# Performance work log

Measured on AMD Instinct MI355X. Metric: run time of the kernel, lower is better.

The kernel has to match this reference:

```python
import jax, jax.numpy as jnp
import numpy as np

NUM_NODES = 512
NUM_EDGES = 512
EMB_DIM = 128
HIDDEN = 256
NUM_INC = 8192


def setup_inputs() -> dict:
    key = jax.random.key(0)
    ks = jax.random.split(key, 8)
    X = jax.random.normal(ks[0], (NUM_NODES, EMB_DIM), dtype=jnp.float32)
    V = jax.random.randint(ks[1], (NUM_INC,), 0, NUM_NODES, dtype=jnp.int64)
    E = jax.random.randint(ks[2], (NUM_INC,), 0, NUM_EDGES, dtype=jnp.int64)
    # MLP params, torch nn.Linear layout: W (out, in), y = x @ W.T + b
    lim1 = 1.0 / np.sqrt(2 * EMB_DIM)
    W1 = jax.random.uniform(ks[3], (HIDDEN, 2 * EMB_DIM), minval=-lim1, maxval=lim1, dtype=jnp.float32)
    b1 = jax.random.uniform(ks[4], (HIDDEN,), minval=-lim1, maxval=lim1, dtype=jnp.float32)
    lim2 = 1.0 / np.sqrt(HIDDEN)
    W2 = jax.random.uniform(ks[5], (1, HIDDEN), minval=-lim2, maxval=lim2, dtype=jnp.float32)
    b2 = jax.random.uniform(ks[6], (1,), minval=-lim2, maxval=lim2, dtype=jnp.float32)
    return {"X": X, "V": V, "E": E, "W1": W1, "b1": b1, "W2": W2, "b2": b2}


def reference(X, V, E, W1, b1, W2, b2):
    d = X.shape[-1]
    # scatter-mean of gathered node embeddings into edges; empty edges -> 0 (nan_to_num)
    sums = jax.ops.segment_sum(X[V], E, num_segments=NUM_EDGES)          # (M, d)
    cnt = jax.ops.segment_sum(jnp.ones((V.shape[0],), X.dtype), E, num_segments=NUM_EDGES)
    eX = jnp.where(cnt[:, None] > 0, sums / jnp.maximum(cnt[:, None], 1.0), 0.0)
    # cat([X_expanded, eX_expanded]) @ W1.T == X @ W1[:, :d].T + eX @ W1[:, d:].T (broadcast add)
    hX = X @ W1[:, :d].T                                                 # (N, H)
    hE = eX @ W1[:, d:].T                                                # (M, H)
    hidden = jax.nn.relu(hX[:, None, :] + hE[None, :, :] + b1)           # (N, M, H)
    logits = jnp.einsum('nmh,h->nm', hidden, W2[0]) + b2[0]              # (N, M)
    prob = jax.nn.sigmoid(logits)
    prob = jnp.nan_to_num(prob, nan=0.5)
    prob = jnp.clip(prob, 1e-6, 1.0 - 1e-6)
    return prob
```

## Files before the change

kernel.cpp:

```cpp
#include <hip/hip_runtime.h>
#include <math.h>

#define NN 512
#define MM 512
#define DD 128
#define HH 256

typedef float     v4f __attribute__((ext_vector_type(4)));
typedef _Float16  h8  __attribute__((ext_vector_type(8)));
typedef _Float16  h2  __attribute__((ext_vector_type(2)));


__global__ __launch_bounds__(256) void k_stage(
    const float* __restrict__ X, const int* __restrict__ V,
    const int* __restrict__ E, const float* __restrict__ W1,
    const float* __restrict__ b1, _Float16* __restrict__ A,
    _Float16* __restrict__ C, int ninc)
{
    __shared__ union {
        int    lst[8192];
        float4 w1t[64][32];
    } u;
    __shared__ float xr[4][128];
    __shared__ float red[16][64];
    __shared__ int   cnt4[4], pos4[4], off4[4];

    const int b = blockIdx.x;
    const int t = threadIdx.x;
    const int w = t >> 6, lane = t & 63;
    const bool edge = (b < 128);

    if (edge) {
        const int e0 = b * 4;
        if (t < 4) { cnt4[t] = 0; pos4[t] = 0; }
        __syncthreads();
        const int nq = ninc >> 2;
        for (int c = t; c < nq; c += 256) {
            int4 e4 = ((const int4*)E)[c];
            if ((unsigned)(e4.x - e0) < 4u) atomicAdd(&cnt4[e4.x - e0], 1);
            if ((unsigned)(e4.y - e0) < 4u) atomicAdd(&cnt4[e4.y - e0], 1);
            if ((unsigned)(e4.z - e0) < 4u) atomicAdd(&cnt4[e4.z - e0], 1);
            if ((unsigned)(e4.w - e0) < 4u) atomicAdd(&cnt4[e4.w - e0], 1);
        }
        __syncthreads();
        if (t == 0) {
            off4[0] = 0;
            off4[1] = cnt4[0];
            off4[2] = cnt4[0] + cnt4[1];
            off4[3] = off4[2] + cnt4[2];
        }
        __syncthreads();
        for (int c = t; c < nq; c += 256) {
            int4 e4 = ((const int4*)E)[c];
            int4 v4 = ((const int4*)V)[c];
            if ((unsigned)(e4.x - e0) < 4u) u.lst[off4[e4.x-e0] + atomicAdd(&pos4[e4.x-e0], 1)] = v4.x;
            if ((unsigned)(e4.y - e0) < 4u) u.lst[off4[e4.y-e0] + atomicAdd(&pos4[e4.y-e0], 1)] = v4.y;
            if ((unsigned)(e4.z - e0) < 4u) u.lst[off4[e4.z-e0] + atomicAdd(&pos4[e4.z-e0], 1)] = v4.z;
            if ((unsigned)(e4.w - e0) < 4u) u.lst[off4[e4.w-e0] + atomicAdd(&pos4[e4.w-e0], 1)] = v4.w;
        }
        __syncthreads();
        const int cnt = cnt4[w], off = off4[w];
        float s0a=0.f,s0b=0.f,s0c=0.f,s0d=0.f, s1a=0.f,s1b=0.f,s1c=0.f,s1d=0.f;
        int j = 0;
        for (; j + 4 <= cnt; j += 4) {
            int v0 = u.lst[off+j], v1 = u.lst[off+j+1], v2 = u.lst[off+j+2], v3 = u.lst[off+j+3];
            s0a += X[v0*DD + lane];      s1a += X[v0*DD + 64 + lane];
            s0b += X[v1*DD + lane];      s1b += X[v1*DD + 64 + lane];
            s0c += X[v2*DD + lane];      s1c += X[v2*DD + 64 + lane];
            s0d += X[v3*DD + lane];      s1d += X[v3*DD + 64 + lane];
        }
        for (; j < cnt; ++j) {
            int v = u.lst[off+j];
            s0a += X[v*DD + lane];       s1a += X[v*DD + 64 + lane];
        }
        float inv = cnt > 0 ? 1.0f / (float)cnt : 0.0f;
        xr[w][lane]      = (s0a+s0b+s0c+s0d) * inv;
        xr[w][lane+64]   = (s1a+s1b+s1c+s1d) * inv;
        __syncthreads();
    } else {
        const int r0 = (b - 128) * 4;
        ((float*)xr)[t]       = X[r0*DD + t];
        ((float*)xr)[t + 256] = X[r0*DD + 256 + t];
        __syncthreads();
    }

    const int r0row = edge ? b*4 : (b-128)*4;
    const int koff  = edge ? DD : 0;
    _Float16* Out   = edge ? C : A;

    #pragma unroll 1
    for (int p = 0; p < 4; ++p) {
        const int h0 = p * 64;
        #pragma unroll
        for (int q = 0; q < 8; ++q) {
            int c  = q * 256 + t;
            int h  = c >> 5, kq = c & 31;
            u.w1t[h][kq ^ (h & 31)] =
                *(const float4*)&W1[(h0 + h) * (2*DD) + koff + kq * 4];
        }
        __syncthreads();
        v4f acc0 = (v4f)(0.f), acc1 = (v4f)(0.f), acc2 = (v4f)(0.f), acc3 = (v4f)(0.f);
        #pragma unroll
        for (int i = 0; i < 8; ++i) {
            int kq = w * 8 + i;
            v4f wv = *(const v4f*)&u.w1t[lane][kq ^ (lane & 31)];
            acc0 += wv * (*(const v4f*)&xr[0][kq*4]);
            acc1 += wv * (*(const v4f*)&xr[1][kq*4]);
            acc2 += wv * (*(const v4f*)&xr[2][kq*4]);
            acc3 += wv * (*(const v4f*)&xr[3][kq*4]);
        }
        red[w*4 + 0][lane] = acc0.x + acc0.y + acc0.z + acc0.w;
        red[w*4 + 1][lane] = acc1.x + acc1.y + acc1.z + acc1.w;
        red[w*4 + 2][lane] = acc2.x + acc2.y + acc2.z + acc2.w;
        red[w*4 + 3][lane] = acc3.x + acc3.y + acc3.z + acc3.w;
        __syncthreads();
        float s = red[w][lane] + red[4 + w][lane] + red[8 + w][lane] + red[12 + w][lane];
        if (edge) s += b1[h0 + lane];
        Out[(r0row + w) * HH + h0 + lane] = (_Float16)s;
        __syncthreads();
    }
}

#define CT 8192
#define WT 16384

__device__ inline float dot8(h8 w, h8 a, h8 c, float acc) {
    h8 s = a + c;
    s = __builtin_elementwise_max(s, (h8)(_Float16)0.f);
    union { h8 v; h2 p[4]; } su, wu;
    su.v = s; wu.v = w;
    acc = __builtin_amdgcn_fdot2(su.p[0], wu.p[0], acc, false);
    acc = __builtin_amdgcn_fdot2(su.p[1], wu.p[1], acc, false);
    acc = __builtin_amdgcn_fdot2(su.p[2], wu.p[2], acc, false);
    acc = __builtin_amdgcn_fdot2(su.p[3], wu.p[3], acc, false);
    return acc;
}

__global__ __launch_bounds__(256) void k_pairs(
    const _Float16* __restrict__ A, const _Float16* __restrict__ C,
    const float* __restrict__ W2, const float* __restrict__ b2,
    float* __restrict__ out)
{
    __shared__ _Float16 lds[WT + 256];
    const int t  = threadIdx.x;
    const int bx = blockIdx.x;
    const int tn0 = (bx >> 4) * 32;
    const int tm0 = (bx & 15) * 32;

    lds[WT + t] = (_Float16)W2[t];
    #pragma unroll
    for (int q = 0; q < 8; ++q) {
        int g   = q * 256 + t;
        int row = g >> 5, cc = g & 31, r = row & 31;
        int dst = (row < 32 ? 0 : CT) + r * 256 + ((cc ^ (r >> 2)) << 3);
        const _Float16* src = (row < 32) ? A + (tn0 + r) * HH + cc * 8
                                         : C + (tm0 + r) * HH + cc * 8;
        *(h8*)&lds[dst] = *(const h8*)src;
    }
    __syncthreads();

    const int w  = t >> 6, lane = t & 63;
    const int qa = lane & 7,  ra = 4 * qa;
    const int qc = lane >> 3, rc = 4 * qc;
    const int h0 = w * 64;

    float acc[4][4];
    #pragma unroll
    for (int i = 0; i < 4; ++i)
        #pragma unroll
        for (int j = 0; j < 4; ++j) acc[i][j] = 0.f;

    #pragma unroll
    for (int hh = 0; hh < 64; hh += 8) {
        int h  = h0 + hh;
        int cc = h >> 3;
        int sa = (cc ^ qa) << 3;
        int sc = (cc ^ qc) << 3;
        h8 wv = *(const h8*)&lds[WT + h];
        h8 av[4], cv[4];
        #pragma unroll
        for (int i = 0; i < 4; ++i) av[i] = *(const h8*)&lds[(ra + i) * 256 + sa];
        #pragma unroll
        for (int j = 0; j < 4; ++j) cv[j] = *(const h8*)&lds[CT + (rc + j) * 256 + sc];
        #pragma unroll
        for (int i = 0; i < 4; ++i)
            #pragma unroll
            for (int j = 0; j < 4; ++j)
                acc[i][j] = dot8(wv, av[i], cv[j], acc[i][j]);
    }

    __syncthreads();
    float* red = (float*)lds;
    #pragma unroll
    for (int i = 0; i < 4; ++i) {
        float4 f;
        f.x = acc[i][0]; f.y = acc[i][1]; f.z = acc[i][2]; f.w = acc[i][3];
        *(float4*)&red[w * 1152 + (ra + i) * 36 + rc] = f;
    }
    __syncthreads();

    const int rr = t >> 3;
    const int c4 = (t & 7) * 4;
    v4f s = *(const v4f*)&red[rr * 36 + c4];
    s += *(const v4f*)&red[1152 + rr * 36 + c4];
    s += *(const v4f*)&red[2304 + rr * 36 + c4];
    s += *(const v4f*)&red[3456 + rr * 36 + c4];
    const float b2v = b2[0];
    float4 o;
    float* op = &o.x;
    #pragma unroll
    for (int k = 0; k < 4; ++k) {
        float logit = s[k] + b2v;
        float p = 1.0f / (1.0f + __expf(-logit));
        op[k] = fminf(fmaxf(p, 1e-6f), 1.0f - 1e-6f);
    }
    *(float4*)&out[(tn0 + rr) * MM + tm0 + c4] = o;
}

extern "C" void kernel_launch(void* const* d_in, const int* in_sizes, int n_in,
                              void* d_out, int out_size, void* d_ws, size_t ws_size,
                              hipStream_t stream)
{
    const float* X  = (const float*)d_in[0];
    const int*   V  = (const int*)d_in[1];
    const int*   E  = (const int*)d_in[2];
    const float* W1 = (const float*)d_in[3];
    const float* b1 = (const float*)d_in[4];
    const float* W2 = (const float*)d_in[5];
    const float* b2 = (const float*)d_in[6];

    _Float16* A = (_Float16*)d_ws;
    _Float16* C = A + NN * HH;
    float* out  = (float*)d_out;
    int ninc    = in_sizes[1];

    k_stage<<<256, 256, 0, stream>>>(X, V, E, W1, b1, A, C, ninc);
    k_pairs<<<256, 256, 0, stream>>>(A, C, W2, b2, out);
}
```

Baseline: 84.66 us.

## Fuse staging and pair kernels into one cooperative launch with grid sync

Merges the projection kernel and the pairwise MLP kernel into a single cooperative kernel, separated by a grid-wide barrier. This removes one kernel launch and the gap between the two kernels. It also replaces the two-pass count-then-scatter bucketing of incidences with a single pass into fixed per-edge lists of 2048 entries. Risks: cooperative launch overhead and grid-sync cost. The fixed-size lists would overflow if one edge ever received more than 2048 incidences.

```diff
diff --git a/kernel.cpp b/kernel.cpp
--- a/kernel.cpp
+++ b/kernel.cpp
@@ -1,5 +1,8 @@
 #include <hip/hip_runtime.h>
+#include <hip/hip_cooperative_groups.h>
 #include <math.h>
+
+namespace cg = cooperative_groups;
 
 #define NN 512
 #define MM 512
@@ -9,117 +12,6 @@
 typedef float     v4f __attribute__((ext_vector_type(4)));
 typedef _Float16  h8  __attribute__((ext_vector_type(8)));
 typedef _Float16  h2  __attribute__((ext_vector_type(2)));
-
-
-__global__ __launch_bounds__(256) void k_stage(
-    const float* __restrict__ X, const int* __restrict__ V,
-    const int* __restrict__ E, const float* __restrict__ W1,
-    const float* __restrict__ b1, _Float16* __restrict__ A,
-    _Float16* __restrict__ C, int ninc)
-{
-    __shared__ union {
-        int    lst[8192];
-        float4 w1t[64][32];
-    } u;
-    __shared__ float xr[4][128];
-    __shared__ float red[16][64];
-    __shared__ int   cnt4[4], pos4[4], off4[4];
-
-    const int b = blockIdx.x;
-    const int t = threadIdx.x;
-    const int w = t >> 6, lane = t & 63;
-    const bool edge = (b < 128);
-
-    if (edge) {
-        const int e0 = b * 4;
-        if (t < 4) { cnt4[t] = 0; pos4[t] = 0; }
-        __syncthreads();
-        const int nq = ninc >> 2;
-        for (int c = t; c < nq; c += 256) {
-            int4 e4 = ((const int4*)E)[c];
-            if ((unsigned)(e4.x - e0) < 4u) atomicAdd(&cnt4[e4.x - e0], 1);
-            if ((unsigned)(e4.y - e0) < 4u) atomicAdd(&cnt4[e4.y - e0], 1);
-            if ((unsigned)(e4.z - e0) < 4u) atomicAdd(&cnt4[e4.z - e0], 1);
-            if ((unsigned)(e4.w - e0) < 4u) atomicAdd(&cnt4[e4.w - e0], 1);
-        }
-        __syncthreads();
-        if (t == 0) {
-            off4[0] = 0;
-            off4[1] = cnt4[0];
-            off4[2] = cnt4[0] + cnt4[1];
-            off4[3] = off4[2] + cnt4[2];
-        }
-        __syncthreads();
-        for (int c = t; c < nq; c += 256) {
-            int4 e4 = ((const int4*)E)[c];
-            int4 v4 = ((const int4*)V)[c];
-            if ((unsigned)(e4.x - e0) < 4u) u.lst[off4[e4.x-e0] + atomicAdd(&pos4[e4.x-e0], 1)] = v4.x;
-            if ((unsigned)(e4.y - e0) < 4u) u.lst[off4[e4.y-e0] + atomicAdd(&pos4[e4.y-e0], 1)] = v4.y;
-            if ((unsigned)(e4.z - e0) < 4u) u.lst[off4[e4.z-e0] + atomicAdd(&pos4[e4.z-e0], 1)] = v4.z;
-            if ((unsigned)(e4.w - e0) < 4u) u.lst[off4[e4.w-e0] + atomicAdd(&pos4[e4.w-e0], 1)] = v4.w;
-        }
-        __syncthreads();
-        const int cnt = cnt4[w], off = off4[w];
-        float s0a=0.f,s0b=0.f,s0c=0.f,s0d=0.f, s1a=0.f,s1b=0.f,s1c=0.f,s1d=0.f;
-        int j = 0;
-        for (; j + 4 <= cnt; j += 4) {
-            int v0 = u.lst[off+j], v1 = u.lst[off+j+1], v2 = u.lst[off+j+2], v3 = u.lst[off+j+3];
-            s0a += X[v0*DD + lane];      s1a += X[v0*DD + 64 + lane];
-            s0b += X[v1*DD + lane];      s1b += X[v1*DD + 64 + lane];
-            s0c += X[v2*DD + lane];      s1c += X[v2*DD + 64 + lane];
-            s0d += X[v3*DD + lane];      s1d += X[v3*DD + 64 + lane];
-        }
-        for (; j < cnt; ++j) {
-            int v = u.lst[off+j];
-            s0a += X[v*DD + lane];       s1a += X[v*DD + 64 + lane];
-        }
-        float inv = cnt > 0 ? 1.0f / (float)cnt : 0.0f;
-        xr[w][lane]      = (s0a+s0b+s0c+s0d) * inv;
-        xr[w][lane+64]   = (s1a+s1b+s1c+s1d) * inv;
-        __syncthreads();
-    } else {
-        const int r0 = (b - 128) * 4;
-        ((float*)xr)[t]       = X[r0*DD + t];
-        ((float*)xr)[t + 256] = X[r0*DD + 256 + t];
-        __syncthreads();
-    }
-
-    const int r0row = edge ? b*4 : (b-128)*4;
-    const int koff  = edge ? DD : 0;
-    _Float16* Out   = edge ? C : A;
-
-    #pragma unroll 1
-    for (int p = 0; p < 4; ++p) {
-        const int h0 = p * 64;
-        #pragma unroll
-        for (int q = 0; q < 8; ++q) {
-            int c  = q * 256 + t;
-            int h  = c >> 5, kq = c & 31;
-            u.w1t[h][kq ^ (h & 31)] =
-                *(const float4*)&W1[(h0 + h) * (2*DD) + koff + kq * 4];
-        }
-        __syncthreads();
-        v4f acc0 = (v4f)(0.f), acc1 = (v4f)(0.f), acc2 = (v4f)(0.f), acc3 = (v4f)(0.f);
-        #pragma unroll
-        for (int i = 0; i < 8; ++i) {
-            int kq = w * 8 + i;
-            v4f wv = *(const v4f*)&u.w1t[lane][kq ^ (lane & 31)];
-            acc0 += wv * (*(const v4f*)&xr[0][kq*4]);
-            acc1 += wv * (*(const v4f*)&xr[1][kq*4]);
-            acc2 += wv * (*(const v4f*)&xr[2][kq*4]);
-            acc3 += wv * (*(const v4f*)&xr[3][kq*4]);
-        }
-        red[w*4 + 0][lane] = acc0.x + acc0.y + acc0.z + acc0.w;
-        red[w*4 + 1][lane] = acc1.x + acc1.y + acc1.z + acc1.w;
-        red[w*4 + 2][lane] = acc2.x + acc2.y + acc2.z + acc2.w;
-        red[w*4 + 3][lane] = acc3.x + acc3.y + acc3.z + acc3.w;
-        __syncthreads();
-        float s = red[w][lane] + red[4 + w][lane] + red[8 + w][lane] + red[12 + w][lane];
-        if (edge) s += b1[h0 + lane];
-        Out[(r0row + w) * HH + h0 + lane] = (_Float16)s;
-        __syncthreads();
-    }
-}
 
 #define CT 8192
 #define WT 16384
@@ -136,85 +28,180 @@
     return acc;
 }
 
-__global__ __launch_bounds__(256) void k_pairs(
-    const _Float16* __restrict__ A, const _Float16* __restrict__ C,
-    const float* __restrict__ W2, const float* __restrict__ b2,
-    float* __restrict__ out)
+__global__ __launch_bounds__(256) void k_fused(
+    const float* __restrict__ X, const int* __restrict__ V,
+    const int* __restrict__ E, const float* __restrict__ W1,
+    const float* __restrict__ b1, const float* __restrict__ W2,
+    const float* __restrict__ b2, _Float16* __restrict__ A,
+    _Float16* __restrict__ C, float* __restrict__ out, int ninc)
 {
-    __shared__ _Float16 lds[WT + 256];
-    const int t  = threadIdx.x;
-    const int bx = blockIdx.x;
-    const int tn0 = (bx >> 4) * 32;
-    const int tm0 = (bx & 15) * 32;
-
-    lds[WT + t] = (_Float16)W2[t];
-    #pragma unroll
-    for (int q = 0; q < 8; ++q) {
-        int g   = q * 256 + t;
-        int row = g >> 5, cc = g & 31, r = row & 31;
-        int dst = (row < 32 ? 0 : CT) + r * 256 + ((cc ^ (r >> 2)) << 3);
-        const _Float16* src = (row < 32) ? A + (tn0 + r) * HH + cc * 8
-                                         : C + (tm0 + r) * HH + cc * 8;
-        *(h8*)&lds[dst] = *(const h8*)src;
+    __shared__ union {
+        int      lst[4][2048];
+        float4   w1t[64][32];
+        _Float16 pt[WT + 256];
+    } u;
+    __shared__ float xr[4][128];
+    __shared__ float red[16][64];
+    __shared__ int   cnt4[4];
+
+    const int b = blockIdx.x;
+    const int t = threadIdx.x;
+    const int w = t >> 6, lane = t & 63;
+    const bool edge = (b < 128);
+
+    if (edge) {
+        const int e0 = b * 4;
+        if (t < 4) cnt4[t] = 0;
+        __syncthreads();
+        const int nq = ninc >> 2;
+        for (int c = t; c < nq; c += 256) {
+            int4 e4 = ((const int4*)E)[c];
+            int4 v4 = ((const int4*)V)[c];
+            int d;
+            d = e4.x - e0; if ((unsigned)d < 4u) u.lst[d][atomicAdd(&cnt4[d], 1)] = v4.x;
+            d = e4.y - e0; if ((unsigned)d < 4u) u.lst[d][atomicAdd(&cnt4[d], 1)] = v4.y;
+            d = e4.z - e0; if ((unsigned)d < 4u) u.lst[d][atomicAdd(&cnt4[d], 1)] = v4.z;
+            d = e4.w - e0; if ((unsigned)d < 4u) u.lst[d][atomicAdd(&cnt4[d], 1)] = v4.w;
+        }
+        __syncthreads();
+        const int cnt = cnt4[w];
+        const int* l  = u.lst[w];
+        float s0a=0.f,s0b=0.f,s0c=0.f,s0d=0.f, s1a=0.f,s1b=0.f,s1c=0.f,s1d=0.f;
+        int j = 0;
+        for (; j + 4 <= cnt; j += 4) {
+            int v0 = l[j], v1 = l[j+1], v2 = l[j+2], v3 = l[j+3];
+            s0a += X[v0*DD + lane];      s1a += X[v0*DD + 64 + lane];
+            s0b += X[v1*DD + lane];      s1b += X[v1*DD + 64 + lane];
+            s0c += X[v2*DD + lane];      s1c += X[v2*DD + 64 + lane];
+            s0d += X[v3*DD + lane];      s1d += X[v3*DD + 64 + lane];
+        }
+        for (; j < cnt; ++j) {
+            int v = l[j];
+            s0a += X[v*DD + lane];       s1a += X[v*DD + 64 + lane];
+        }
+        float inv = cnt > 0 ? 1.0f / (float)cnt : 0.0f;
+        xr[w][lane]    = (s0a+s0b+s0c+s0d) * inv;
+        xr[w][lane+64] = (s1a+s1b+s1c+s1d) * inv;
+        __syncthreads();
+    } else {
+        const int r0 = (b - 128) * 4;
+        ((float*)xr)[t]       = X[r0*DD + t];
+        ((float*)xr)[t + 256] = X[r0*DD + 256 + t];
+        __syncthreads();
     }
-    __syncthreads();
-
-    const int w  = t >> 6, lane = t & 63;
-    const int qa = lane & 7,  ra = 4 * qa;
-    const int qc = lane >> 3, rc = 4 * qc;
-    const int h0 = w * 64;
-
-    float acc[4][4];
-    #pragma unroll
-    for (int i = 0; i < 4; ++i)
-        #pragma unroll
-        for (int j = 0; j < 4; ++j) acc[i][j] = 0.f;
-
-    #pragma unroll
-    for (int hh = 0; hh < 64; hh += 8) {
-        int h  = h0 + hh;
-        int cc = h >> 3;
-        int sa = (cc ^ qa) << 3;
-        int sc = (cc ^ qc) << 3;
-        h8 wv = *(const h8*)&lds[WT + h];
-        h8 av[4], cv[4];
-        #pragma unroll
-        for (int i = 0; i < 4; ++i) av[i] = *(const h8*)&lds[(ra + i) * 256 + sa];
-        #pragma unroll
-        for (int j = 0; j < 4; ++j) cv[j] = *(const h8*)&lds[CT + (rc + j) * 256 + sc];
+
+    {
+        const int r0row = edge ? b*4 : (b-128)*4;
+        const int koff  = edge ? DD : 0;
+        _Float16* Out   = edge ? C : A;
+
+        #pragma unroll 1
+        for (int p = 0; p < 4; ++p) {
+            const int h0 = p * 64;
+            #pragma unroll
+            for (int q = 0; q < 8; ++q) {
+                int c  = q * 256 + t;
+                int h  = c >> 5, kq = c & 31;
+                u.w1t[h][kq ^ (h & 31)] =
+                    *(const float4*)&W1[(h0 + h) * (2*DD) + koff + kq * 4];
+            }
+            __syncthreads();
+            v4f acc0 = (v4f)(0.f), acc1 = (v4f)(0.f), acc2 = (v4f)(0.f), acc3 = (v4f)(0.f);
+            #pragma unroll
+            for (int i = 0; i < 8; ++i) {
+                int kq = w * 8 + i;
+                v4f wv = *(const v4f*)&u.w1t[lane][kq ^ (lane & 31)];
+                acc0 += wv * (*(const v4f*)&xr[0][kq*4]);
+                acc1 += wv * (*(const v4f*)&xr[1][kq*4]);
+                acc2 += wv * (*(const v4f*)&xr[2][kq*4]);
+                acc3 += wv * (*(const v4f*)&xr[3][kq*4]);
+            }
+            red[w*4 + 0][lane] = acc0.x + acc0.y + acc0.z + acc0.w;
+            red[w*4 + 1][lane] = acc1.x + acc1.y + acc1.z + acc1.w;
+            red[w*4 + 2][lane] = acc2.x + acc2.y + acc2.z + acc2.w;
+            red[w*4 + 3][lane] = acc3.x + acc3.y + acc3.z + acc3.w;
+            __syncthreads();
+            float s = red[w][lane] + red[4 + w][lane] + red[8 + w][lane] + red[12 + w][lane];
+            if (edge) s += b1[h0 + lane];
+            Out[(r0row + w) * HH + h0 + lane] = (_Float16)s;
+            __syncthreads();
+        }
+    }
+
+    cg::this_grid().sync();
+
+    {
+        const int tn0 = (b >> 4) * 32;
+        const int tm0 = (b & 15) * 32;
+
+        u.pt[WT + t] = (_Float16)W2[t];
+        #pragma unroll
+        for (int q = 0; q < 8; ++q) {
+            int g   = q * 256 + t;
+            int row = g >> 5, cc = g & 31, r = row & 31;
+            int dst = (row < 32 ? 0 : CT) + r * 256 + ((cc ^ (r >> 2)) << 3);
+            const _Float16* src = (row < 32) ? A + (tn0 + r) * HH + cc * 8
+                                             : C + (tm0 + r) * HH + cc * 8;
+            *(h8*)&u.pt[dst] = *(const h8*)src;
+        }
+        __syncthreads();
+
+        const int qa = lane & 7,  ra = 4 * qa;
+        const int qc = lane >> 3, rc = 4 * qc;
+        const int h0 = w * 64;
+
+        float acc[4][4];
         #pragma unroll
         for (int i = 0; i < 4; ++i)
             #pragma unroll
-            for (int j = 0; j < 4; ++j)
-                acc[i][j] = dot8(wv, av[i], cv[j], acc[i][j]);
+            for (int j = 0; j < 4; ++j) acc[i][j] = 0.f;
+
+        #pragma unroll
+        for (int hh = 0; hh < 64; hh += 8) {
+            int h  = h0 + hh;
+            int cc = h >> 3;
+            int sa = (cc ^ qa) << 3;
+            int sc = (cc ^ qc) << 3;
+            h8 wv = *(const h8*)&u.pt[WT + h];
+            h8 av[4], cv[4];
+            #pragma unroll
+            for (int i = 0; i < 4; ++i) av[i] = *(const h8*)&u.pt[(ra + i) * 256 + sa];
+            #pragma unroll
+            for (int j = 0; j < 4; ++j) cv[j] = *(const h8*)&u.pt[CT + (rc + j) * 256 + sc];
+            #pragma unroll
+            for (int i = 0; i < 4; ++i)
+                #pragma unroll
+                for (int j = 0; j < 4; ++j)
+                    acc[i][j] = dot8(wv, av[i], cv[j], acc[i][j]);
+        }
+
+        __syncthreads();
+        float* red2 = (float*)u.pt;
+        #pragma unroll
+        for (int i = 0; i < 4; ++i) {
+            float4 f;
+            f.x = acc[i][0]; f.y = acc[i][1]; f.z = acc[i][2]; f.w = acc[i][3];
+            *(float4*)&red2[w * 1152 + (ra + i) * 36 + rc] = f;
+        }
+        __syncthreads();
+
+        const int rr = t >> 3;
+        const int c4 = (t & 7) * 4;
+        v4f s = *(const v4f*)&red2[rr * 36 + c4];
+        s += *(const v4f*)&red2[1152 + rr * 36 + c4];
+        s += *(const v4f*)&red2[2304 + rr * 36 + c4];
+        s += *(const v4f*)&red2[3456 + rr * 36 + c4];
+        const float b2v = b2[0];
+        float4 o;
+        float* op = &o.x;
+        #pragma unroll
+        for (int k = 0; k < 4; ++k) {
+            float logit = s[k] + b2v;
+            float p = 1.0f / (1.0f + __expf(-logit));
+            op[k] = fminf(fmaxf(p, 1e-6f), 1.0f - 1e-6f);
+        }
+        *(float4*)&out[(tn0 + rr) * MM + tm0 + c4] = o;
     }
-
-    __syncthreads();
-    float* red = (float*)lds;
-    #pragma unroll
-    for (int i = 0; i < 4; ++i) {
-        float4 f;
-        f.x = acc[i][0]; f.y = acc[i][1]; f.z = acc[i][2]; f.w = acc[i][3];
-        *(float4*)&red[w * 1152 + (ra + i) * 36 + rc] = f;
-    }
-    __syncthreads();
-
-    const int rr = t >> 3;
-    const int c4 = (t & 7) * 4;
-    v4f s = *(const v4f*)&red[rr * 36 + c4];
-    s += *(const v4f*)&red[1152 + rr * 36 + c4];
-    s += *(const v4f*)&red[2304 + rr * 36 + c4];
-    s += *(const v4f*)&red[3456 + rr * 36 + c4];
-    const float b2v = b2[0];
-    float4 o;
-    float* op = &o.x;
-    #pragma unroll
-    for (int k = 0; k < 4; ++k) {
-        float logit = s[k] + b2v;
-        float p = 1.0f / (1.0f + __expf(-logit));
-        op[k] = fminf(fmaxf(p, 1e-6f), 1.0f - 1e-6f);
-    }
-    *(float4*)&out[(tn0 + rr) * MM + tm0 + c4] = o;
 }
 
 extern "C" void kernel_launch(void* const* d_in, const int* in_sizes, int n_in,
@@ -234,6 +221,8 @@
     float* out  = (float*)d_out;
     int ninc    = in_sizes[1];
 
-    k_stage<<<256, 256, 0, stream>>>(X, V, E, W1, b1, A, C, ninc);
-    k_pairs<<<256, 256, 0, stream>>>(A, C, W2, b2, out);
+    void* args[] = {(void*)&X, (void*)&V, (void*)&E, (void*)&W1, (void*)&b1,
+                    (void*)&W2, (void*)&b2, (void*)&A, (void*)&C, (void*)&out,
+                    (void*)&ninc};
+    hipLaunchCooperativeKernel((void*)k_fused, dim3(256), dim3(256), args, 0, stream);
 }
```

Result: slower. 124.7 us (+47.2%).
